# Kernel optimization log

Measured on AMD Instinct MI355X. Metric: run time of the kernel, lower is better.

The kernel has to match this reference:

```python
import jax, jax.numpy as jnp
import numpy as np

WS = 8          # window size (== stride, non-overlapping)
C_IN = 256
RED = 8
C_QK = C_IN // RED  # 32


def setup_inputs() -> dict:
    key = jax.random.key(0)
    ks = jax.random.split(key, 8)
    B, C, H, W = 4, C_IN, 256, 256
    x = jax.random.normal(ks[0], (B, C, H, W), dtype=jnp.float32)
    # 1x1 conv weights stored as [out_ch, in_ch] (kaiming-ish scale)
    wq = jax.random.normal(ks[1], (C_QK, C), dtype=jnp.float32) * np.sqrt(2.0 / C)
    wk = jax.random.normal(ks[2], (C_QK, C), dtype=jnp.float32) * np.sqrt(2.0 / C)
    wv = jax.random.normal(ks[3], (C, C), dtype=jnp.float32) * np.sqrt(2.0 / C)
    bq = jnp.zeros((C_QK,), dtype=jnp.float32)
    bk = jnp.zeros((C_QK,), dtype=jnp.float32)
    bv = jnp.zeros((C,), dtype=jnp.float32)
    gamma = jax.random.normal(ks[4], (1,), dtype=jnp.float32) * 0.5
    return {"x": x, "wq": wq, "bq": bq, "wk": wk, "bk": bk,
            "wv": wv, "bv": bv, "gamma": gamma}


def reference(x, wq, bq, wk, bk, wv, bv, gamma):
    B, C, H, W = x.shape
    Hw, Ww = H // WS, W // WS
    P = WS * WS  # 64 pixels per window
    # extract non-overlapping windows: [B,C,H,W] -> [N, C, P]
    xw = x.reshape(B, C, Hw, WS, Ww, WS)
    xw = xw.transpose(0, 2, 4, 1, 3, 5).reshape(B * Hw * Ww, C, P)
    # 1x1 conv projections (per-pixel channel GEMM)
    q = jnp.einsum('ncp,oc->nop', xw, wq) + bq[None, :, None]   # [N, Cqk, P]
    k = jnp.einsum('ncp,oc->nop', xw, wk) + bk[None, :, None]   # [N, Cqk, P]
    v = jnp.einsum('ncp,oc->nop', xw, wv) + bv[None, :, None]   # [N, C,   P]
    # attn[p, q_] = <Q[:,p], K[:,q_]> / sqrt(P), softmax over q_
    scale = 1.0 / np.sqrt(float(P))
    attn = jax.nn.softmax(jnp.einsum('ncp,ncq->npq', q, k) * scale, axis=-1)
    # out = V @ attn^T : out[c,p] = sum_q V[c,q] * attn[p,q]
    out = jnp.einsum('ncq,npq->ncp', v, attn)  # [N, C, P]
    # merge windows back: [N, C, P] -> [B, C, H, W]
    out = out.reshape(B, Hw, Ww, C, WS, WS)
    out = out.transpose(0, 3, 1, 4, 2, 5).reshape(B, C, H, W)
    return gamma * out + x
```

## Files before the change

kernel.cpp:

```cpp
#include <hip/hip_runtime.h>
#include <hip/hip_bf16.h>
#include <stdint.h>


#define CIN    256
#define WIMG   256
#define CH_STRIDE 65536

typedef __bf16 bf16x8 __attribute__((ext_vector_type(8)));
typedef float  f32x4  __attribute__((ext_vector_type(4)));

#define XT_OFF 0
#define QT_OFF 32768
#define KT_OFF 36864
#define PT_OFF 32768
#define LDS_BYTES 40960

__device__ __forceinline__ int swz8(int p) { return (p ^ (p >> 3)) & 7; }

__device__ __forceinline__ uint32_t pack2(float lo, float hi) {
  union { __bf16 h[2]; uint32_t u; } un;
  un.h[0] = (__bf16)lo; un.h[1] = (__bf16)hi;
  return un.u;
}

union fragu { uint32_t u[4]; bf16x8 v; };

__global__ __launch_bounds__(256) void wprep_kernel(
    const float* __restrict__ wq, const float* __restrict__ wk,
    const float* __restrict__ wv, __bf16* __restrict__ out)
{
  int i = blockIdx.x * 256 + threadIdx.x;
  int off = i * 4;
  const float* src;
  if (off < 8192)       src = wq + off;
  else if (off < 16384) src = wk + (off - 8192);
  else                  src = wv + (off - 16384);
  float4 v = *(const float4*)src;
  __bf16 h[4] = {(__bf16)v.x, (__bf16)v.y, (__bf16)v.z, (__bf16)v.w};
  *(uint2*)(out + off) = *(const uint2*)h;
}

__global__ __launch_bounds__(256, 4) void win_attn_kernel(
    const float* __restrict__ x,  const __bf16* __restrict__ wsb,
    const float* __restrict__ bq, const float* __restrict__ bk,
    const float* __restrict__ bv, const float* __restrict__ gamma,
    float* __restrict__ out, int nwin)
{
  __shared__ __attribute__((aligned(16))) unsigned char lds[LDS_BYTES];

  int bid   = blockIdx.x;
  int chunk = nwin >> 3;
  int swz   = (bid & 7) * chunk + (bid >> 3);
  int b  = swz >> 10;
  int hw = (swz >> 5) & 31;
  int ww = swz & 31;
  size_t win_off = (size_t)b * (CIN * CH_STRIDE) + (size_t)hw * 8 * WIMG + (size_t)ww * 8;
  const float* xw = x + win_off;
  float* ow = out + win_off;

  int t = threadIdx.x;
  int w = t >> 6, l = t & 63, l16 = l & 15, lq = l >> 4;
  float g = gamma[0];

  float bvv[4];
  #pragma unroll
  for (int ci = 0; ci < 4; ++ci) bvv[ci] = bv[w * 64 + ci * 16 + l16];

  int qkrow = (w & 1) * 16;
  bf16x8 wqkf[8];
  {
    const __bf16* qrow = wsb + ((w < 2) ? 0 : 8192) + (qkrow + l16) * 256 + lq * 8;
    #pragma unroll
    for (int ks = 0; ks < 8; ++ks) wqkf[ks] = *(const bf16x8*)(qrow + ks * 32);
  }

  #pragma unroll
  for (int it = 0; it < 8; ++it) {
    int id   = it * 256 + t;
    int half = id & 1;
    int i    = (id >> 1) & 7;
    int c2   = id >> 4;
    const float* r0 = xw + (size_t)(2 * c2) * CH_STRIDE + i * WIMG + half * 4;
    float4 va = *(const float4*)r0;
    float4 vb = *(const float4*)(r0 + CH_STRIDE);
    float ax[4] = {va.x, va.y, va.z, va.w};
    float bx[4] = {vb.x, vb.y, vb.z, vb.w};
    int blk = c2 >> 2;
    int sub = (c2 & 3) * 4;
    #pragma unroll
    for (int jj = 0; jj < 4; ++jj) {
      int p = i * 8 + half * 4 + jj;
      *(uint32_t*)(lds + XT_OFF + p * 512 + ((blk ^ swz8(p)) << 4) + sub) =
          pack2(ax[jj], bx[jj]);
    }
  }
  __syncthreads();

  {
    f32x4 qacc[4] = {};
    #pragma unroll
    for (int ks = 0; ks < 8; ++ks) {
      bf16x8 xb[4];
      #pragma unroll
      for (int qi = 0; qi < 4; ++qi) {
        int p = qi * 16 + l16;
        xb[qi] = *(const bf16x8*)(lds + XT_OFF + p * 512 +
                                  (((ks * 4 + lq) ^ swz8(p)) << 4));
      }
      #pragma unroll
      for (int qi = 0; qi < 4; ++qi)
        qacc[qi] = __builtin_amdgcn_mfma_f32_16x16x32_bf16(wqkf[ks], xb[qi], qacc[qi], 0, 0, 0);
    }
    const float* bias = (w < 2) ? bq : bk;
    int lbase = (w < 2) ? QT_OFF : KT_OFF;
    #pragma unroll
    for (int r = 0; r < 4; ++r) {
      int c = qkrow + lq * 4 + r;
      float bb = bias[c];
      #pragma unroll
      for (int qi = 0; qi < 4; ++qi) {
        int p = qi * 16 + l16;
        *(__bf16*)(lds + lbase + p * 64 + (((c >> 3) ^ (p & 3)) << 4) + (c & 7) * 2) =
            (__bf16)(qacc[qi][r] + bb);
      }
    }
  }
  __syncthreads();

  uint32_t dP[4][2];
  {
    int pq = w * 16 + l16;
    bf16x8 qa = *(const bf16x8*)(lds + QT_OFF + pq * 64 + ((lq ^ (pq & 3)) << 4));
    f32x4 sacc[4];
    #pragma unroll
    for (int qi = 0; qi < 4; ++qi) {
      int pk = qi * 16 + l16;
      bf16x8 kb = *(const bf16x8*)(lds + KT_OFF + pk * 64 + ((lq ^ (pk & 3)) << 4));
      f32x4 z = {0.f, 0.f, 0.f, 0.f};
      sacc[qi] = __builtin_amdgcn_mfma_f32_16x16x32_bf16(kb, qa, z, 0, 0, 0);
    }
    float e[4][4];
    float mx = -1e30f;
    #pragma unroll
    for (int qi = 0; qi < 4; ++qi)
      #pragma unroll
      for (int r = 0; r < 4; ++r) {
        float v = sacc[qi][r] * 0.125f;
        e[qi][r] = v;
        mx = fmaxf(mx, v);
      }
    mx = fmaxf(mx, __shfl_xor(mx, 16));
    mx = fmaxf(mx, __shfl_xor(mx, 32));
    float s = 0.f;
    #pragma unroll
    for (int qi = 0; qi < 4; ++qi)
      #pragma unroll
      for (int r = 0; r < 4; ++r) {
        e[qi][r] = __expf(e[qi][r] - mx);
        s += e[qi][r];
      }
    s += __shfl_xor(s, 16);
    s += __shfl_xor(s, 32);
    float inv = 1.0f / s;
    #pragma unroll
    for (int qi = 0; qi < 4; ++qi) {
      dP[qi][0] = pack2(e[qi][0] * inv, e[qi][1] * inv);
      dP[qi][1] = pack2(e[qi][2] * inv, e[qi][3] * inv);
    }
  }

  uint32_t dV[4][4][2];
  {
    f32x4 vacc[4][4] = {};
    const __bf16* vrow = wsb + 16384 + (w * 64 + l16) * 256 + lq * 8;
    #pragma unroll
    for (int ks = 0; ks < 8; ++ks) {
      bf16x8 xb[4];
      #pragma unroll
      for (int pi = 0; pi < 4; ++pi) {
        int p = pi * 16 + l16;
        xb[pi] = *(const bf16x8*)(lds + XT_OFF + p * 512 +
                                  (((ks * 4 + lq) ^ swz8(p)) << 4));
      }
      #pragma unroll
      for (int ci = 0; ci < 4; ++ci) {
        bf16x8 wvf = *(const bf16x8*)(vrow + ci * 16 * 256 + ks * 32);
        #pragma unroll
        for (int pi = 0; pi < 4; ++pi)
          vacc[pi][ci] = __builtin_amdgcn_mfma_f32_16x16x32_bf16(xb[pi], wvf, vacc[pi][ci], 0, 0, 0);
      }
    }
    #pragma unroll
    for (int pi = 0; pi < 4; ++pi)
      #pragma unroll
      for (int ci = 0; ci < 4; ++ci) {
        dV[pi][ci][0] = pack2(vacc[pi][ci][0], vacc[pi][ci][1]);
        dV[pi][ci][1] = pack2(vacc[pi][ci][2], vacc[pi][ci][3]);
      }
  }
  __syncthreads();

  {
    int q = w * 16 + l16;
    int qm = q & 7;
    #pragma unroll
    for (int qi = 0; qi < 4; ++qi) {
      int blk = (((qi >> 1) * 4) + lq) ^ qm;
      uint2 val; val.x = dP[qi][0]; val.y = dP[qi][1];
      *(uint2*)(lds + PT_OFF + q * 128 + blk * 16 + (qi & 1) * 8) = val;
    }
  }
  __syncthreads();

  f32x4 oacc[4][4] = {};
  #pragma unroll
  for (int ks = 0; ks < 2; ++ks) {
    bf16x8 Pf[4];
    #pragma unroll
    for (int bj = 0; bj < 4; ++bj) {
      int q = bj * 16 + l16;
      int blk = (ks * 4 + lq) ^ (q & 7);
      Pf[bj] = *(const bf16x8*)(lds + PT_OFF + q * 128 + blk * 16);
    }
    #pragma unroll
    for (int ci = 0; ci < 4; ++ci) {
      fragu Vf;
      Vf.u[0] = dV[2 * ks][ci][0];
      Vf.u[1] = dV[2 * ks][ci][1];
      Vf.u[2] = dV[2 * ks + 1][ci][0];
      Vf.u[3] = dV[2 * ks + 1][ci][1];
      #pragma unroll
      for (int bj = 0; bj < 4; ++bj)
        oacc[ci][bj] = __builtin_amdgcn_mfma_f32_16x16x32_bf16(Pf[bj], Vf.v, oacc[ci][bj], 0, 0, 0);
    }
  }

  #pragma unroll
  for (int ci = 0; ci < 4; ++ci) {
    int c = w * 64 + ci * 16 + l16;
    size_t cbase = (size_t)c * CH_STRIDE;
    float bvc = bvv[ci];
    int chi = c >> 3, clo = (c & 7) * 2;
    #pragma unroll
    for (int bj = 0; bj < 4; ++bj) {
      int p0 = bj * 16 + lq * 4;
      float xr[4];
      #pragma unroll
      for (int r = 0; r < 4; ++r) {
        int p = p0 + r;
        xr[r] = (float)(*(const __bf16*)(lds + XT_OFF + p * 512 +
                                         ((chi ^ swz8(p)) << 4) + clo));
      }
      float4 o;
      o.x = g * (oacc[ci][bj][0] + bvc) + xr[0];
      o.y = g * (oacc[ci][bj][1] + bvc) + xr[1];
      o.z = g * (oacc[ci][bj][2] + bvc) + xr[2];
      o.w = g * (oacc[ci][bj][3] + bvc) + xr[3];
      *(float4*)(ow + cbase + (size_t)(p0 >> 3) * WIMG + (p0 & 7)) = o;
    }
  }
}

extern "C" void kernel_launch(void* const* d_in, const int* in_sizes, int n_in,
                              void* d_out, int out_size, void* d_ws, size_t ws_size,
                              hipStream_t stream) {
  const float* x     = (const float*)d_in[0];
  const float* wq    = (const float*)d_in[1];
  const float* bq    = (const float*)d_in[2];
  const float* wk    = (const float*)d_in[3];
  const float* bk    = (const float*)d_in[4];
  const float* wv    = (const float*)d_in[5];
  const float* bv    = (const float*)d_in[6];
  const float* gamma = (const float*)d_in[7];
  float* out = (float*)d_out;
  __bf16* wsb = (__bf16*)d_ws;

  wprep_kernel<<<dim3(80), dim3(256), 0, stream>>>(wq, wk, wv, wsb);

  int B = in_sizes[0] / (CIN * CH_STRIDE);
  int nwin = B * 1024;
  win_attn_kernel<<<dim3(nwin), dim3(256), 0, stream>>>(
      x, wsb, bq, bk, bv, gamma, out, nwin);
}
```

Baseline: 272.4 us.

## Process two horizontally adjacent windows per 512-thread block

Each block now has 512 threads, and each 256-thread half handles one of two horizontally adjacent windows, using its own slice of dynamic LDS (2x40KB). The aim is better coalescing of the x loads and output stores across neighbouring windows, and fewer block launches. The Wv fragment loads are hoisted ahead of the LDS reads in each k-step, and the bv load moves to the epilogue to save registers. In exchange, __syncthreads now covers both windows, launch_bounds drops the occupancy hint, and the larger LDS footprint per block may limit how many blocks fit on a CU.

```diff
diff --git a/kernel.cpp b/kernel.cpp
--- a/kernel.cpp
+++ b/kernel.cpp
@@ -14,7 +14,7 @@
 #define QT_OFF 32768
 #define KT_OFF 36864
 #define PT_OFF 32768
-#define LDS_BYTES 40960
+#define HALF_LDS 40960
 
 __device__ __forceinline__ int swz8(int p) { return (p ^ (p >> 3)) & 7; }
 
@@ -41,31 +41,32 @@
   *(uint2*)(out + off) = *(const uint2*)h;
 }
 
-__global__ __launch_bounds__(256, 4) void win_attn_kernel(
+__global__ __launch_bounds__(512) void win_attn_kernel(
     const float* __restrict__ x,  const __bf16* __restrict__ wsb,
     const float* __restrict__ bq, const float* __restrict__ bk,
     const float* __restrict__ bv, const float* __restrict__ gamma,
-    float* __restrict__ out, int nwin)
+    float* __restrict__ out, int nblk)
 {
-  __shared__ __attribute__((aligned(16))) unsigned char lds[LDS_BYTES];
+  extern __shared__ __attribute__((aligned(16))) unsigned char lds_raw[];
+
+  int t = threadIdx.x;
+  int half = t >> 8;
+  int tt = t & 255;
+  unsigned char* ldsb = lds_raw + half * HALF_LDS;
 
   int bid   = blockIdx.x;
-  int chunk = nwin >> 3;
+  int chunk = nblk >> 3;
   int swz   = (bid & 7) * chunk + (bid >> 3);
-  int b  = swz >> 10;
-  int hw = (swz >> 5) & 31;
-  int ww = swz & 31;
+  int b   = swz >> 9;
+  int hw  = (swz >> 4) & 31;
+  int wwp = swz & 15;
+  int ww  = wwp * 2 + half;
   size_t win_off = (size_t)b * (CIN * CH_STRIDE) + (size_t)hw * 8 * WIMG + (size_t)ww * 8;
   const float* xw = x + win_off;
   float* ow = out + win_off;
 
-  int t = threadIdx.x;
-  int w = t >> 6, l = t & 63, l16 = l & 15, lq = l >> 4;
+  int w = tt >> 6, l = tt & 63, l16 = l & 15, lq = l >> 4;
   float g = gamma[0];
-
-  float bvv[4];
-  #pragma unroll
-  for (int ci = 0; ci < 4; ++ci) bvv[ci] = bv[w * 64 + ci * 16 + l16];
 
   int qkrow = (w & 1) * 16;
   bf16x8 wqkf[8];
@@ -77,11 +78,11 @@
 
   #pragma unroll
   for (int it = 0; it < 8; ++it) {
-    int id   = it * 256 + t;
-    int half = id & 1;
+    int id   = it * 256 + tt;
+    int hf   = id & 1;
     int i    = (id >> 1) & 7;
     int c2   = id >> 4;
-    const float* r0 = xw + (size_t)(2 * c2) * CH_STRIDE + i * WIMG + half * 4;
+    const float* r0 = xw + (size_t)(2 * c2) * CH_STRIDE + i * WIMG + hf * 4;
     float4 va = *(const float4*)r0;
     float4 vb = *(const float4*)(r0 + CH_STRIDE);
     float ax[4] = {va.x, va.y, va.z, va.w};
@@ -90,8 +91,8 @@
     int sub = (c2 & 3) * 4;
     #pragma unroll
     for (int jj = 0; jj < 4; ++jj) {
-      int p = i * 8 + half * 4 + jj;
-      *(uint32_t*)(lds + XT_OFF + p * 512 + ((blk ^ swz8(p)) << 4) + sub) =
+      int p = i * 8 + hf * 4 + jj;
+      *(uint32_t*)(ldsb + XT_OFF + p * 512 + ((blk ^ swz8(p)) << 4) + sub) =
           pack2(ax[jj], bx[jj]);
     }
   }
@@ -105,7 +106,7 @@
       #pragma unroll
       for (int qi = 0; qi < 4; ++qi) {
         int p = qi * 16 + l16;
-        xb[qi] = *(const bf16x8*)(lds + XT_OFF + p * 512 +
+        xb[qi] = *(const bf16x8*)(ldsb + XT_OFF + p * 512 +
                                   (((ks * 4 + lq) ^ swz8(p)) << 4));
       }
       #pragma unroll
@@ -121,7 +122,7 @@
       #pragma unroll
       for (int qi = 0; qi < 4; ++qi) {
         int p = qi * 16 + l16;
-        *(__bf16*)(lds + lbase + p * 64 + (((c >> 3) ^ (p & 3)) << 4) + (c & 7) * 2) =
+        *(__bf16*)(ldsb + lbase + p * 64 + (((c >> 3) ^ (p & 3)) << 4) + (c & 7) * 2) =
             (__bf16)(qacc[qi][r] + bb);
       }
     }
@@ -131,12 +132,12 @@
   uint32_t dP[4][2];
   {
     int pq = w * 16 + l16;
-    bf16x8 qa = *(const bf16x8*)(lds + QT_OFF + pq * 64 + ((lq ^ (pq & 3)) << 4));
+    bf16x8 qa = *(const bf16x8*)(ldsb + QT_OFF + pq * 64 + ((lq ^ (pq & 3)) << 4));
     f32x4 sacc[4];
     #pragma unroll
     for (int qi = 0; qi < 4; ++qi) {
       int pk = qi * 16 + l16;
-      bf16x8 kb = *(const bf16x8*)(lds + KT_OFF + pk * 64 + ((lq ^ (pk & 3)) << 4));
+      bf16x8 kb = *(const bf16x8*)(ldsb + KT_OFF + pk * 64 + ((lq ^ (pk & 3)) << 4));
       f32x4 z = {0.f, 0.f, 0.f, 0.f};
       sacc[qi] = __builtin_amdgcn_mfma_f32_16x16x32_bf16(kb, qa, z, 0, 0, 0);
     }
@@ -176,19 +177,22 @@
     const __bf16* vrow = wsb + 16384 + (w * 64 + l16) * 256 + lq * 8;
     #pragma unroll
     for (int ks = 0; ks < 8; ++ks) {
+      bf16x8 wvf[4];
+      #pragma unroll
+      for (int ci = 0; ci < 4; ++ci)
+        wvf[ci] = *(const bf16x8*)(vrow + ci * 16 * 256 + ks * 32);
       bf16x8 xb[4];
       #pragma unroll
       for (int pi = 0; pi < 4; ++pi) {
         int p = pi * 16 + l16;
-        xb[pi] = *(const bf16x8*)(lds + XT_OFF + p * 512 +
+        xb[pi] = *(const bf16x8*)(ldsb + XT_OFF + p * 512 +
                                   (((ks * 4 + lq) ^ swz8(p)) << 4));
       }
       #pragma unroll
       for (int ci = 0; ci < 4; ++ci) {
-        bf16x8 wvf = *(const bf16x8*)(vrow + ci * 16 * 256 + ks * 32);
         #pragma unroll
         for (int pi = 0; pi < 4; ++pi)
-          vacc[pi][ci] = __builtin_amdgcn_mfma_f32_16x16x32_bf16(xb[pi], wvf, vacc[pi][ci], 0, 0, 0);
+          vacc[pi][ci] = __builtin_amdgcn_mfma_f32_16x16x32_bf16(xb[pi], wvf[ci], vacc[pi][ci], 0, 0, 0);
       }
     }
     #pragma unroll
@@ -208,7 +212,7 @@
     for (int qi = 0; qi < 4; ++qi) {
       int blk = (((qi >> 1) * 4) + lq) ^ qm;
       uint2 val; val.x = dP[qi][0]; val.y = dP[qi][1];
-      *(uint2*)(lds + PT_OFF + q * 128 + blk * 16 + (qi & 1) * 8) = val;
+      *(uint2*)(ldsb + PT_OFF + q * 128 + blk * 16 + (qi & 1) * 8) = val;
     }
   }
   __syncthreads();
@@ -221,7 +225,7 @@
     for (int bj = 0; bj < 4; ++bj) {
       int q = bj * 16 + l16;
       int blk = (ks * 4 + lq) ^ (q & 7);
-      Pf[bj] = *(const bf16x8*)(lds + PT_OFF + q * 128 + blk * 16);
+      Pf[bj] = *(const bf16x8*)(ldsb + PT_OFF + q * 128 + blk * 16);
     }
     #pragma unroll
     for (int ci = 0; ci < 4; ++ci) {
@@ -240,7 +244,7 @@
   for (int ci = 0; ci < 4; ++ci) {
     int c = w * 64 + ci * 16 + l16;
     size_t cbase = (size_t)c * CH_STRIDE;
-    float bvc = bvv[ci];
+    float bvc = bv[c];
     int chi = c >> 3, clo = (c & 7) * 2;
     #pragma unroll
     for (int bj = 0; bj < 4; ++bj) {
@@ -249,7 +253,7 @@
       #pragma unroll
       for (int r = 0; r < 4; ++r) {
         int p = p0 + r;
-        xr[r] = (float)(*(const __bf16*)(lds + XT_OFF + p * 512 +
+        xr[r] = (float)(*(const __bf16*)(ldsb + XT_OFF + p * 512 +
                                          ((chi ^ swz8(p)) << 4) + clo));
       }
       float4 o;
@@ -276,10 +280,13 @@
   float* out = (float*)d_out;
   __bf16* wsb = (__bf16*)d_ws;
 
+  hipFuncSetAttribute((const void*)win_attn_kernel,
+                      hipFuncAttributeMaxDynamicSharedMemorySize, 2 * HALF_LDS);
+
   wprep_kernel<<<dim3(80), dim3(256), 0, stream>>>(wq, wk, wv, wsb);
 
   int B = in_sizes[0] / (CIN * CH_STRIDE);
-  int nwin = B * 1024;
-  win_attn_kernel<<<dim3(nwin), dim3(256), 0, stream>>>(
-      x, wsb, bq, bk, bv, gamma, out, nwin);
-}
+  int nblk = B * 512;
+  win_attn_kernel<<<dim3(nblk), dim3(512), 2 * HALF_LDS, stream>>>(
+      x, wsb, bq, bk, bv, gamma, out, nblk);
+}
```

After: 255.4 us. 1.07x faster.
